# Kernel optimization log

Measured on AMD Instinct MI355X. Metric: run time of the kernel, lower is better.

Reference implementation:

```python
import jax, jax.numpy as jnp
import numpy as np

N = 8192
F = 512
H = 256
O = 128
C = 64
E = 262144


def gcn_conv(x, W, b, src, dst, num_nodes):
    # PyG GCNConv: h = XW; add self-loops; symmetric deg^{-1/2} normalization; scatter-add; + bias
    h = x @ W  # [N, out]
    deg = jnp.zeros((num_nodes,), h.dtype).at[dst].add(1.0) + 1.0  # self-loop included
    dinv = jax.lax.rsqrt(deg)
    norm = (dinv[src] * dinv[dst])[:, None]  # [E, 1]
    agg = jnp.zeros_like(h).at[dst].add(h[src] * norm)
    agg = agg + h * (1.0 / deg)[:, None]  # self-loop contribution: deg^{-1/2} * deg^{-1/2}
    return agg + b


def setup_inputs() -> dict:
    key = jax.random.key(0)
    ks = jax.random.split(key, 12)
    x = jax.random.normal(ks[0], (N, F), jnp.float32)
    edge_index = jax.random.randint(ks[1], (2, E), 0, N, jnp.int64)
    eps = jax.random.normal(ks[2], (N, C), jnp.float32)
    s1 = 1.0 / np.sqrt(F)
    s2 = 1.0 / np.sqrt(H)
    s3 = 1.0 / np.sqrt(O)
    W1 = jax.random.uniform(ks[3], (F, H), jnp.float32, -s1, s1)
    b1 = jnp.zeros((H,), jnp.float32)
    W2 = jax.random.uniform(ks[4], (H, O), jnp.float32, -s2, s2)
    b2 = jnp.zeros((O,), jnp.float32)
    Wmu = jax.random.uniform(ks[5], (O, C), jnp.float32, -s3, s3)
    bmu = jax.random.uniform(ks[6], (C,), jnp.float32, -s3, s3)
    Wlv = jax.random.uniform(ks[7], (O, C), jnp.float32, -s3, s3)
    blv = jax.random.uniform(ks[8], (C,), jnp.float32, -s3, s3)
    return {"x": x, "edge_index": edge_index, "eps": eps,
            "W1": W1, "b1": b1, "W2": W2, "b2": b2,
            "Wmu": Wmu, "bmu": bmu, "Wlv": Wlv, "blv": blv}


def reference(x, edge_index, eps, W1, b1, W2, b2, Wmu, bmu, Wlv, blv):
    src, dst = edge_index[0], edge_index[1]
    n = x.shape[0]
    h = jax.nn.relu(gcn_conv(x, W1, b1, src, dst, n))
    z = gcn_conv(h, W2, b2, src, dst, n)  # [N, O]
    mu = z @ Wmu + bmu       # [N, C]
    logvar = z @ Wlv + blv   # [N, C]
    std = jnp.exp(0.5 * logvar)
    zr = mu + eps * std      # reparameterize
    adj_recon = jax.nn.sigmoid(zr @ zr.T)  # [N, N]
    return (adj_recon, mu, logvar)
```

## Files before the change

### kernel.cpp

```cpp
#include <hip/hip_runtime.h>
#include <hip/hip_bf16.h>

#define N_NODES 8192
#define F_IN    512
#define H_DIM   256
#define O_DIM   128
#define C_DIM   64
#define E_EDGES 262144
#define BCAP    96

typedef __attribute__((ext_vector_type(8))) short bf16x8;
typedef __attribute__((ext_vector_type(8))) _Float16 f16x8;
typedef __attribute__((ext_vector_type(4))) float f32x4;

__device__ inline unsigned short f2bf(float v) {
    __hip_bfloat16 h = __float2bfloat16(v);
    return *reinterpret_cast<unsigned short*>(&h);
}
__device__ inline float bf2f(unsigned short u) {
    return __uint_as_float((unsigned)u << 16);
}
__device__ inline void split2(float v, unsigned short& hi, unsigned short& lo) {
    hi = f2bf(v);
    lo = f2bf(v - bf2f(hi));
}
__device__ inline float4 bf4_to_f4(ushort4 u) {
    float4 f;
    f.x = bf2f(u.x); f.y = bf2f(u.y); f.z = bf2f(u.z); f.w = bf2f(u.w);
    return f;
}

__global__ __launch_bounds__(256) void prep_kernel(
    const float* __restrict__ x, unsigned short* __restrict__ xb,
    const float* __restrict__ W1, unsigned short* __restrict__ w1t,
    const float* __restrict__ W2, unsigned short* __restrict__ w2th, unsigned short* __restrict__ w2tl,
    int* __restrict__ cnt)
{
    const int NX4 = N_NODES * F_IN / 4;
    const int NW1 = F_IN * H_DIM;
    const int NW2 = H_DIM * O_DIM;
    int idx = blockIdx.x * 256 + threadIdx.x;
    if (idx < N_NODES) cnt[idx] = 0;
    if (idx < NX4) {
        float4 v = ((const float4*)x)[idx];
        ushort4 b;
        b.x = f2bf(v.x); b.y = f2bf(v.y); b.z = f2bf(v.z); b.w = f2bf(v.w);
        ((ushort4*)xb)[idx] = b;
    } else if (idx < NX4 + NW1) {
        int j = idx - NX4;
        int k = j / H_DIM, n = j % H_DIM;
        w1t[n * F_IN + k] = f2bf(W1[j]);
    } else if (idx < NX4 + NW1 + NW2) {
        int j = idx - NX4 - NW1;
        int k = j / O_DIM, n = j % O_DIM;
        unsigned short h, l;
        split2(W2[j], h, l);
        w2th[n * H_DIM + k] = h;
        w2tl[n * H_DIM + k] = l;
    }
}

__global__ __launch_bounds__(256) void gemm1_kernel(
    const unsigned short* __restrict__ xb,
    const unsigned short* __restrict__ Bt,
    const int* __restrict__ srcv, const int* __restrict__ dstv,
    int* __restrict__ cnt, int* __restrict__ slots,
    unsigned short* __restrict__ out)
{
    {
        int flat = (blockIdx.y * gridDim.x + blockIdx.x) * 256 + threadIdx.x;
        int e0 = flat * 2;
#pragma unroll
        for (int j = 0; j < 2; ++j) {
            int d = dstv[e0 + j];
            int pos = atomicAdd(&cnt[d], 1);
            slots[d * BCAP + pos] = srcv[e0 + j];
        }
    }

    constexpr int N = H_DIM, K = F_IN, MW = 2, NW = 2;
    const int tid = threadIdx.x;
    const int lane = tid & 63;
    const int wid = tid >> 6;
    const int r = lane & 15;
    const int kg = lane >> 4;
    const int m0 = blockIdx.y * (2 * MW * 16) + (wid >> 1) * (MW * 16);
    const int n0 = blockIdx.x * (2 * NW * 16) + (wid & 1) * (NW * 16);

    f32x4 acc[MW][NW];
#pragma unroll
    for (int mi = 0; mi < MW; ++mi)
#pragma unroll
        for (int ni = 0; ni < NW; ++ni) acc[mi][ni] = (f32x4){0.f, 0.f, 0.f, 0.f};

    for (int k0 = 0; k0 < K; k0 += 32) {
        const int kof = k0 + kg * 8;
        bf16x8 a[MW], b[NW];
#pragma unroll
        for (int mi = 0; mi < MW; ++mi)
            a[mi] = *(const bf16x8*)(xb + (size_t)(m0 + mi * 16 + r) * K + kof);
#pragma unroll
        for (int ni = 0; ni < NW; ++ni)
            b[ni] = *(const bf16x8*)(Bt + (size_t)(n0 + ni * 16 + r) * K + kof);
#pragma unroll
        for (int mi = 0; mi < MW; ++mi)
#pragma unroll
            for (int ni = 0; ni < NW; ++ni)
                acc[mi][ni] = __builtin_amdgcn_mfma_f32_16x16x32_bf16(a[mi], b[ni], acc[mi][ni], 0, 0, 0);
    }

#pragma unroll
    for (int mi = 0; mi < MW; ++mi) {
        int rowb = m0 + mi * 16 + kg * 4;
#pragma unroll
        for (int ni = 0; ni < NW; ++ni) {
            int col = n0 + ni * 16 + r;
#pragma unroll
            for (int i = 0; i < 4; ++i)
                out[(size_t)(rowb + i) * N + col] = f2bf(acc[mi][ni][i]);
        }
    }
}

__global__ __launch_bounds__(256) void gather_gemm2_kernel(
    const unsigned short* __restrict__ raw,
    const int* __restrict__ cnt, const int* __restrict__ slots,
    const float* __restrict__ b1,
    const unsigned short* __restrict__ w2th, const unsigned short* __restrict__ w2tl,
    unsigned short* __restrict__ g2b)
{
    __shared__ unsigned short hs[16 * 256];
    const int tid = threadIdx.x;
    const int wid = tid >> 6;
    const int lane = tid & 63;
    const int nb = blockIdx.x * 16;
    const ushort4* G4 = (const ushort4*)raw;

    for (int q = 0; q < 4; ++q) {
        const int ln = wid * 4 + q;
        const int node = nb + ln;
        const int deg = cnt[node];
        const int* sl = slots + node * BCAP;
        const float di = rsqrtf((float)deg + 1.0f);

        float4 selfv = bf4_to_f4(G4[(size_t)node * 64 + lane]);
        float4 acc, acc2;
        acc.x = di * selfv.x; acc.y = di * selfv.y;
        acc.z = di * selfv.z; acc.w = di * selfv.w;
        acc2 = make_float4(0.f, 0.f, 0.f, 0.f);

        int e = 0;
        for (; e + 8 <= deg; e += 8) {
            int s[8];
            ushort4 u[8];
            float d[8];
#pragma unroll
            for (int j = 0; j < 8; ++j) s[j] = sl[e + j];
#pragma unroll
            for (int j = 0; j < 8; ++j) u[j] = G4[(size_t)s[j] * 64 + lane];
#pragma unroll
            for (int j = 0; j < 8; ++j) d[j] = rsqrtf((float)cnt[s[j]] + 1.0f);
#pragma unroll
            for (int j = 0; j < 8; j += 2) {
                float4 v0 = bf4_to_f4(u[j]);
                float4 v1 = bf4_to_f4(u[j + 1]);
                acc.x = fmaf(d[j], v0.x, acc.x);     acc.y = fmaf(d[j], v0.y, acc.y);
                acc.z = fmaf(d[j], v0.z, acc.z);     acc.w = fmaf(d[j], v0.w, acc.w);
                acc2.x = fmaf(d[j+1], v1.x, acc2.x); acc2.y = fmaf(d[j+1], v1.y, acc2.y);
                acc2.z = fmaf(d[j+1], v1.z, acc2.z); acc2.w = fmaf(d[j+1], v1.w, acc2.w);
            }
        }
        for (; e < deg; ++e) {
            int s0 = sl[e];
            float d0 = rsqrtf((float)cnt[s0] + 1.0f);
            float4 v0 = bf4_to_f4(G4[(size_t)s0 * 64 + lane]);
            acc.x = fmaf(d0, v0.x, acc.x); acc.y = fmaf(d0, v0.y, acc.y);
            acc.z = fmaf(d0, v0.z, acc.z); acc.w = fmaf(d0, v0.w, acc.w);
        }
        acc.x += acc2.x; acc.y += acc2.y; acc.z += acc2.z; acc.w += acc2.w;

        const float4 bv = ((const float4*)b1)[lane];
        float4 rr;
        rr.x = di * acc.x + bv.x;
        rr.y = di * acc.y + bv.y;
        rr.z = di * acc.z + bv.z;
        rr.w = di * acc.w + bv.w;
        rr.x = rr.x > 0.f ? rr.x : 0.f;
        rr.y = rr.y > 0.f ? rr.y : 0.f;
        rr.z = rr.z > 0.f ? rr.z : 0.f;
        rr.w = rr.w > 0.f ? rr.w : 0.f;

        ushort4 hv;
        hv.x = f2bf(rr.x); hv.y = f2bf(rr.y); hv.z = f2bf(rr.z); hv.w = f2bf(rr.w);
        int s0 = (lane >> 1) ^ (ln & 7);
        *(ushort4*)((char*)hs + ln * 512 + (s0 << 4) + (lane & 1) * 8) = hv;
    }
    __syncthreads();

    const int r = lane & 15;
    const int kg = lane >> 4;
    const int wn = wid * 32;

    f32x4 acc[2];
    acc[0] = (f32x4){0.f, 0.f, 0.f, 0.f};
    acc[1] = (f32x4){0.f, 0.f, 0.f, 0.f};

    for (int k0 = 0; k0 < H_DIM; k0 += 32) {
        int slot = ((k0 >> 3) + kg) ^ (r & 7);
        bf16x8 a = *(const bf16x8*)((const char*)hs + r * 512 + (slot << 4));
#pragma unroll
        for (int ni = 0; ni < 2; ++ni) {
            size_t off = (size_t)(wn + ni * 16 + r) * H_DIM + k0 + kg * 8;
            bf16x8 bh = *(const bf16x8*)(w2th + off);
            bf16x8 bl = *(const bf16x8*)(w2tl + off);
            acc[ni] = __builtin_amdgcn_mfma_f32_16x16x32_bf16(a, bh, acc[ni], 0, 0, 0);
            acc[ni] = __builtin_amdgcn_mfma_f32_16x16x32_bf16(a, bl, acc[ni], 0, 0, 0);
        }
    }

    float di4[4];
#pragma unroll
    for (int i = 0; i < 4; ++i) di4[i] = rsqrtf((float)cnt[nb + kg * 4 + i] + 1.0f);
#pragma unroll
    for (int ni = 0; ni < 2; ++ni) {
#pragma unroll
        for (int i = 0; i < 4; ++i) {
            int row = nb + kg * 4 + i;
            g2b[(size_t)row * O_DIM + wn + ni * 16 + r] = f2bf(di4[i] * acc[ni][i]);
        }
    }
}

__global__ __launch_bounds__(128) void gather_head_kernel(
    const unsigned short* __restrict__ g2,
    const int* __restrict__ cnt, const int* __restrict__ slots,
    const float* __restrict__ b2,
    const float* __restrict__ Wmu, const float* __restrict__ bmu,
    const float* __restrict__ Wlv, const float* __restrict__ blv,
    const float* __restrict__ eps,
    float* __restrict__ mu_out, float* __restrict__ lv_out,
    _Float16* __restrict__ zr)
{
    __shared__ float zsw[2][O_DIM];
    __shared__ float zs[O_DIM];
    __shared__ float mu_s[C_DIM];
    __shared__ float lv_s[C_DIM];
    const int node = blockIdx.x;
    const int t = threadIdx.x;
    const int w = t >> 6;
    const int lane = t & 63;

    const int deg = cnt[node];
    const int* sl = slots + node * BCAP;
    const unsigned int* G2 = (const unsigned int*)g2;

    float a0 = 0.f, a1 = 0.f, c0 = 0.f, c1 = 0.f;
    if (w == 0) {
        unsigned int u = G2[(size_t)node * 64 + lane];
        a0 = bf2f((unsigned short)u);
        a1 = bf2f((unsigned short)(u >> 16));
    }
    int e = w;
    for (; e + 6 < deg; e += 8) {
        unsigned int u0 = G2[(size_t)sl[e]     * 64 + lane];
        unsigned int u1 = G2[(size_t)sl[e + 2] * 64 + lane];
        unsigned int u2 = G2[(size_t)sl[e + 4] * 64 + lane];
        unsigned int u3 = G2[(size_t)sl[e + 6] * 64 + lane];
        a0 += bf2f((unsigned short)u0) + bf2f((unsigned short)u1);
        a1 += bf2f((unsigned short)(u0 >> 16)) + bf2f((unsigned short)(u1 >> 16));
        c0 += bf2f((unsigned short)u2) + bf2f((unsigned short)u3);
        c1 += bf2f((unsigned short)(u2 >> 16)) + bf2f((unsigned short)(u3 >> 16));
    }
    for (; e < deg; e += 2) {
        unsigned int u = G2[(size_t)sl[e] * 64 + lane];
        a0 += bf2f((unsigned short)u);
        a1 += bf2f((unsigned short)(u >> 16));
    }
    zsw[w][2 * lane]     = a0 + c0;
    zsw[w][2 * lane + 1] = a1 + c1;
    __syncthreads();

    float dv = rsqrtf((float)deg + 1.0f);
    zs[t] = dv * (zsw[0][t] + zsw[1][t]) + b2[t];
    __syncthreads();

    const int c = t & 63;
    const float* W = (t < 64) ? Wmu : Wlv;
    float s = 0.f;
#pragma unroll 8
    for (int k = 0; k < O_DIM; ++k) s += zs[k] * W[k * C_DIM + c];
    if (t < 64) {
        s += bmu[c];
        mu_out[(size_t)node * C_DIM + c] = s;
        mu_s[c] = s;
    } else {
        s += blv[c];
        lv_out[(size_t)node * C_DIM + c] = s;
        lv_s[c] = s;
    }
    __syncthreads();
    if (t < 64) {
        float stdv = __expf(0.5f * lv_s[c]);
        float v = mu_s[c] + eps[(size_t)node * C_DIM + c] * stdv;
        zr[(size_t)node * C_DIM + c] = (_Float16)v;
    }
}

__global__ __launch_bounds__(256) void adj_mfma_kernel(
    const _Float16* __restrict__ Z, float* __restrict__ out)
{
    const int tid = threadIdx.x;
    const int lane = tid & 63;
    const int wid = tid >> 6;
    const int r = lane & 15;
    const int kg = lane >> 4;
    const int m0 = blockIdx.y * 128 + (wid >> 1) * 64;
    const int n0 = blockIdx.x * 128 + (wid & 1) * 64;

    f16x8 a[4][2], b[4][2];
#pragma unroll
    for (int mi = 0; mi < 4; ++mi)
#pragma unroll
        for (int ks = 0; ks < 2; ++ks) {
            a[mi][ks] = *(const f16x8*)(Z + (size_t)(m0 + mi * 16 + r) * C_DIM + ks * 32 + kg * 8);
            b[mi][ks] = *(const f16x8*)(Z + (size_t)(n0 + mi * 16 + r) * C_DIM + ks * 32 + kg * 8);
        }

    f32x4 acc[4][4];
#pragma unroll
    for (int mi = 0; mi < 4; ++mi)
#pragma unroll
        for (int ni = 0; ni < 4; ++ni) acc[mi][ni] = (f32x4){0.f, 0.f, 0.f, 0.f};

#pragma unroll
    for (int mi = 0; mi < 4; ++mi)
#pragma unroll
        for (int ni = 0; ni < 4; ++ni) {
            acc[mi][ni] = __builtin_amdgcn_mfma_f32_16x16x32_f16(a[mi][0], b[ni][0], acc[mi][ni], 0, 0, 0);
            acc[mi][ni] = __builtin_amdgcn_mfma_f32_16x16x32_f16(a[mi][1], b[ni][1], acc[mi][ni], 0, 0, 0);
        }

#pragma unroll
    for (int mi = 0; mi < 4; ++mi) {
        int rowb = m0 + mi * 16 + kg * 4;
#pragma unroll
        for (int ni = 0; ni < 4; ++ni) {
            int col = n0 + ni * 16 + r;
#pragma unroll
            for (int i = 0; i < 4; ++i) {
                float v = acc[mi][ni][i];
                float e = __expf(-v);
                float sg = __builtin_amdgcn_rcpf(1.0f + e);
                __builtin_nontemporal_store(sg, &out[(size_t)(rowb + i) * N_NODES + col]);
            }
        }
    }
}

extern "C" void kernel_launch(void* const* d_in, const int* in_sizes, int n_in,
                              void* d_out, int out_size, void* d_ws, size_t ws_size,
                              hipStream_t stream) {
    const float* x   = (const float*)d_in[0];
    const int*   ei  = (const int*)  d_in[1];
    const float* eps = (const float*)d_in[2];
    const float* W1  = (const float*)d_in[3];
    const float* b1  = (const float*)d_in[4];
    const float* W2  = (const float*)d_in[5];
    const float* b2  = (const float*)d_in[6];
    const float* Wmu = (const float*)d_in[7];
    const float* bmu = (const float*)d_in[8];
    const float* Wlv = (const float*)d_in[9];
    const float* blv = (const float*)d_in[10];
    float* out = (float*)d_out;

    const int* srcv = ei;
    const int* dstv = ei + E_EDGES;

    char* p = (char*)d_ws;
    auto carve = [&](size_t bytes) -> void* {
        void* q = (void*)p;
        p += (bytes + 255) & ~(size_t)255;
        return q;
    };
    int* cnt      = (int*)carve(N_NODES * 4);
    int* slots    = (int*)carve((size_t)N_NODES * BCAP * 4);
    unsigned short* xb   = (unsigned short*)carve((size_t)N_NODES * F_IN * 2);
    unsigned short* w1t  = (unsigned short*)carve((size_t)F_IN * H_DIM * 2);
    unsigned short* w2th = (unsigned short*)carve((size_t)H_DIM * O_DIM * 2);
    unsigned short* w2tl = (unsigned short*)carve((size_t)H_DIM * O_DIM * 2);
    unsigned short* raw1 = (unsigned short*)carve((size_t)N_NODES * H_DIM * 2);
    unsigned short* g2b  = (unsigned short*)carve((size_t)N_NODES * O_DIM * 2);
    _Float16* zr         = (_Float16*)carve((size_t)N_NODES * C_DIM * 2);

    float* mu_out = out + (size_t)N_NODES * N_NODES;
    float* lv_out = mu_out + (size_t)N_NODES * C_DIM;

    {
        const int total = N_NODES * F_IN / 4 + F_IN * H_DIM + H_DIM * O_DIM;
        prep_kernel<<<(total + 255) / 256, 256, 0, stream>>>(
            x, xb, W1, w1t, W2, w2th, w2tl, cnt);
    }

    {
        dim3 grid(H_DIM / 64, N_NODES / 64);
        gemm1_kernel<<<grid, 256, 0, stream>>>(
            xb, w1t, srcv, dstv, cnt, slots, raw1);
    }

    gather_gemm2_kernel<<<N_NODES / 16, 256, 0, stream>>>(
        raw1, cnt, slots, b1, w2th, w2tl, g2b);

    gather_head_kernel<<<N_NODES, 128, 0, stream>>>(
        g2b, cnt, slots, b2, Wmu, bmu, Wlv, blv, eps,
        mu_out, lv_out, zr);

    {
        dim3 grid(N_NODES / 128, N_NODES / 128);
        adj_mfma_kernel<<<grid, 256, 0, stream>>>(zr, out);
    }
}
```

Measured before the change: 173.7 us.

## Convert x to bf16 inside GEMM1, drop W2 hi/lo split, widen gather block

The separate pass that converted x to bf16 is removed. GEMM1 now loads fp32 x directly and packs it to bf16 in registers, which saves a 16 MB write and reread. The W2 hi/lo bf16 split is replaced by a single bf16 copy, halving GEMM2's MFMA work and weight loads at some cost in precision. The gather+GEMM2 kernel moves to 512 threads, so each wave gathers 2 nodes and computes one 16-column tile, raising parallelism in the gather phase.

```diff
diff --git a/kernel.cpp b/kernel.cpp
--- a/kernel.cpp
+++ b/kernel.cpp
@@ -20,48 +20,41 @@
 __device__ inline float bf2f(unsigned short u) {
     return __uint_as_float((unsigned)u << 16);
 }
-__device__ inline void split2(float v, unsigned short& hi, unsigned short& lo) {
-    hi = f2bf(v);
-    lo = f2bf(v - bf2f(hi));
-}
 __device__ inline float4 bf4_to_f4(ushort4 u) {
     float4 f;
     f.x = bf2f(u.x); f.y = bf2f(u.y); f.z = bf2f(u.z); f.w = bf2f(u.w);
     return f;
 }
+__device__ inline bf16x8 pack_bf8(float4 a, float4 b) {
+    bf16x8 r;
+    r[0] = (short)f2bf(a.x); r[1] = (short)f2bf(a.y);
+    r[2] = (short)f2bf(a.z); r[3] = (short)f2bf(a.w);
+    r[4] = (short)f2bf(b.x); r[5] = (short)f2bf(b.y);
+    r[6] = (short)f2bf(b.z); r[7] = (short)f2bf(b.w);
+    return r;
+}
 
 __global__ __launch_bounds__(256) void prep_kernel(
-    const float* __restrict__ x, unsigned short* __restrict__ xb,
     const float* __restrict__ W1, unsigned short* __restrict__ w1t,
-    const float* __restrict__ W2, unsigned short* __restrict__ w2th, unsigned short* __restrict__ w2tl,
+    const float* __restrict__ W2, unsigned short* __restrict__ w2t,
     int* __restrict__ cnt)
 {
-    const int NX4 = N_NODES * F_IN / 4;
     const int NW1 = F_IN * H_DIM;
     const int NW2 = H_DIM * O_DIM;
     int idx = blockIdx.x * 256 + threadIdx.x;
     if (idx < N_NODES) cnt[idx] = 0;
-    if (idx < NX4) {
-        float4 v = ((const float4*)x)[idx];
-        ushort4 b;
-        b.x = f2bf(v.x); b.y = f2bf(v.y); b.z = f2bf(v.z); b.w = f2bf(v.w);
-        ((ushort4*)xb)[idx] = b;
-    } else if (idx < NX4 + NW1) {
-        int j = idx - NX4;
-        int k = j / H_DIM, n = j % H_DIM;
-        w1t[n * F_IN + k] = f2bf(W1[j]);
-    } else if (idx < NX4 + NW1 + NW2) {
-        int j = idx - NX4 - NW1;
+    if (idx < NW1) {
+        int k = idx / H_DIM, n = idx % H_DIM;
+        w1t[n * F_IN + k] = f2bf(W1[idx]);
+    } else if (idx < NW1 + NW2) {
+        int j = idx - NW1;
         int k = j / O_DIM, n = j % O_DIM;
-        unsigned short h, l;
-        split2(W2[j], h, l);
-        w2th[n * H_DIM + k] = h;
-        w2tl[n * H_DIM + k] = l;
+        w2t[n * H_DIM + k] = f2bf(W2[j]);
     }
 }
 
 __global__ __launch_bounds__(256) void gemm1_kernel(
-    const unsigned short* __restrict__ xb,
+    const float* __restrict__ x,
     const unsigned short* __restrict__ Bt,
     const int* __restrict__ srcv, const int* __restrict__ dstv,
     int* __restrict__ cnt, int* __restrict__ slots,
@@ -97,8 +90,12 @@
         const int kof = k0 + kg * 8;
         bf16x8 a[MW], b[NW];
 #pragma unroll
-        for (int mi = 0; mi < MW; ++mi)
-            a[mi] = *(const bf16x8*)(xb + (size_t)(m0 + mi * 16 + r) * K + kof);
+        for (int mi = 0; mi < MW; ++mi) {
+            const float* xr = x + (size_t)(m0 + mi * 16 + r) * K + kof;
+            float4 f0 = *(const float4*)xr;
+            float4 f1 = *(const float4*)(xr + 4);
+            a[mi] = pack_bf8(f0, f1);
+        }
 #pragma unroll
         for (int ni = 0; ni < NW; ++ni)
             b[ni] = *(const bf16x8*)(Bt + (size_t)(n0 + ni * 16 + r) * K + kof);
@@ -122,11 +119,11 @@
     }
 }
 
-__global__ __launch_bounds__(256) void gather_gemm2_kernel(
+__global__ __launch_bounds__(512) void gather_gemm2_kernel(
     const unsigned short* __restrict__ raw,
     const int* __restrict__ cnt, const int* __restrict__ slots,
     const float* __restrict__ b1,
-    const unsigned short* __restrict__ w2th, const unsigned short* __restrict__ w2tl,
+    const unsigned short* __restrict__ w2t,
     unsigned short* __restrict__ g2b)
 {
     __shared__ unsigned short hs[16 * 256];
@@ -136,8 +133,8 @@
     const int nb = blockIdx.x * 16;
     const ushort4* G4 = (const ushort4*)raw;
 
-    for (int q = 0; q < 4; ++q) {
-        const int ln = wid * 4 + q;
+    for (int q = 0; q < 2; ++q) {
+        const int ln = wid * 2 + q;
         const int node = nb + ln;
         const int deg = cnt[node];
         const int* sl = slots + node * BCAP;
@@ -199,35 +196,21 @@
 
     const int r = lane & 15;
     const int kg = lane >> 4;
-    const int wn = wid * 32;
-
-    f32x4 acc[2];
-    acc[0] = (f32x4){0.f, 0.f, 0.f, 0.f};
-    acc[1] = (f32x4){0.f, 0.f, 0.f, 0.f};
-
+    const int wn = wid * 16;
+
+    f32x4 acc = (f32x4){0.f, 0.f, 0.f, 0.f};
     for (int k0 = 0; k0 < H_DIM; k0 += 32) {
         int slot = ((k0 >> 3) + kg) ^ (r & 7);
         bf16x8 a = *(const bf16x8*)((const char*)hs + r * 512 + (slot << 4));
-#pragma unroll
-        for (int ni = 0; ni < 2; ++ni) {
-            size_t off = (size_t)(wn + ni * 16 + r) * H_DIM + k0 + kg * 8;
-            bf16x8 bh = *(const bf16x8*)(w2th + off);
-            bf16x8 bl = *(const bf16x8*)(w2tl + off);
-            acc[ni] = __builtin_amdgcn_mfma_f32_16x16x32_bf16(a, bh, acc[ni], 0, 0, 0);
-            acc[ni] = __builtin_amdgcn_mfma_f32_16x16x32_bf16(a, bl, acc[ni], 0, 0, 0);
-        }
-    }
-
-    float di4[4];
-#pragma unroll
-    for (int i = 0; i < 4; ++i) di4[i] = rsqrtf((float)cnt[nb + kg * 4 + i] + 1.0f);
-#pragma unroll
-    for (int ni = 0; ni < 2; ++ni) {
-#pragma unroll
-        for (int i = 0; i < 4; ++i) {
-            int row = nb + kg * 4 + i;
-            g2b[(size_t)row * O_DIM + wn + ni * 16 + r] = f2bf(di4[i] * acc[ni][i]);
-        }
+        bf16x8 b = *(const bf16x8*)(w2t + (size_t)(wn + r) * H_DIM + k0 + kg * 8);
+        acc = __builtin_amdgcn_mfma_f32_16x16x32_bf16(a, b, acc, 0, 0, 0);
+    }
+
+#pragma unroll
+    for (int i = 0; i < 4; ++i) {
+        int row = nb + kg * 4 + i;
+        float di = rsqrtf((float)cnt[row] + 1.0f);
+        g2b[(size_t)row * O_DIM + wn + r] = f2bf(di * acc[i]);
     }
 }
 
@@ -384,10 +367,8 @@
     };
     int* cnt      = (int*)carve(N_NODES * 4);
     int* slots    = (int*)carve((size_t)N_NODES * BCAP * 4);
-    unsigned short* xb   = (unsigned short*)carve((size_t)N_NODES * F_IN * 2);
     unsigned short* w1t  = (unsigned short*)carve((size_t)F_IN * H_DIM * 2);
-    unsigned short* w2th = (unsigned short*)carve((size_t)H_DIM * O_DIM * 2);
-    unsigned short* w2tl = (unsigned short*)carve((size_t)H_DIM * O_DIM * 2);
+    unsigned short* w2t  = (unsigned short*)carve((size_t)H_DIM * O_DIM * 2);
     unsigned short* raw1 = (unsigned short*)carve((size_t)N_NODES * H_DIM * 2);
     unsigned short* g2b  = (unsigned short*)carve((size_t)N_NODES * O_DIM * 2);
     _Float16* zr         = (_Float16*)carve((size_t)N_NODES * C_DIM * 2);
@@ -396,19 +377,19 @@
     float* lv_out = mu_out + (size_t)N_NODES * C_DIM;
 
     {
-        const int total = N_NODES * F_IN / 4 + F_IN * H_DIM + H_DIM * O_DIM;
+        const int total = F_IN * H_DIM + H_DIM * O_DIM;
         prep_kernel<<<(total + 255) / 256, 256, 0, stream>>>(
-            x, xb, W1, w1t, W2, w2th, w2tl, cnt);
+            W1, w1t, W2, w2t, cnt);
     }
 
     {
         dim3 grid(H_DIM / 64, N_NODES / 64);
         gemm1_kernel<<<grid, 256, 0, stream>>>(
-            xb, w1t, srcv, dstv, cnt, slots, raw1);
-    }
-
-    gather_gemm2_kernel<<<N_NODES / 16, 256, 0, stream>>>(
-        raw1, cnt, slots, b1, w2th, w2tl, g2b);
+            x, w1t, srcv, dstv, cnt, slots, raw1);
+    }
+
+    gather_gemm2_kernel<<<N_NODES / 16, 512, 0, stream>>>(
+        raw1, cnt, slots, b1, w2t, g2b);
 
     gather_head_kernel<<<N_NODES, 128, 0, stream>>>(
         g2b, cnt, slots, b2, Wmu, bmu, Wlv, blv, eps,
```

After: 166.3 us. 1.04x faster.
